# Optimization experiments

Hardware: AMD Instinct MI355X
Metric: run time of the kernel (lower is better)

The kernel has to match this reference:

```python
import jax, jax.numpy as jnp
import numpy as np

B, S, D, H, L, V = 2, 1024, 512, 8, 4, 32000
DK = D // H
EPS = 1e-6


def _positional_encoding():
    # row i of the original (d_model, seq) array: sin if i even else cos of t/10000^(2i/D); transposed -> (S, D)
    i = jnp.arange(D, dtype=jnp.float32)
    ang = jnp.arange(S, dtype=jnp.float32)[:, None] / (10000.0 ** (2.0 * i / D))[None, :]
    return jnp.where((jnp.arange(D) % 2 == 0)[None, :], jnp.sin(ang), jnp.cos(ang))


def _layernorm(x, g, b):
    m = jnp.mean(x, axis=-1, keepdims=True)
    s = jnp.std(x, axis=-1, keepdims=True)
    return g / (s + EPS) * (x - m) + b


def _mha(x, wq, wk, wv, wo, mask):
    # wq/wk/wv: [H, D, DK]; all heads batched via einsum (equivalent to per-head loop + concat)
    q = jnp.einsum('bsd,hdk->bhsk', x, wq)
    k = jnp.einsum('bsd,hdk->bhsk', x, wk)
    v = jnp.einsum('bsd,hdk->bhsk', x, wv)
    scores = jnp.einsum('bhsk,bhtk->bhst', q, k) / np.float32(np.sqrt(DK))
    if mask is not None:
        scores = scores + mask  # additive upper-tri 1e-15, faithful to source
    attn = jax.nn.softmax(scores, axis=-1)
    o = jnp.einsum('bhst,bhtv->bhsv', attn, v)
    o = o.transpose(0, 2, 1, 3).reshape(B, S, D)  # concat heads
    return o @ wo


def setup_inputs() -> dict:
    key = jax.random.key(0)
    ks = jax.random.split(key, 13)
    n = lambda k, shape, s=0.05: jax.random.normal(k, shape, dtype=jnp.float32) * s
    return {
        'tokens': jax.random.randint(ks[0], (B, S), 0, V),
        'emb': n(ks[1], (V, D)),
        'Wq': n(ks[2], (L, 2, H, D, DK)),
        'Wk': n(ks[3], (L, 2, H, D, DK)),
        'Wv': n(ks[4], (L, 2, H, D, DK)),
        'Wo': n(ks[5], (L, 2, D, D)),
        'ln_gain': 1.0 + n(ks[6], (L, 3, S, D)),
        'ln_bias': n(ks[7], (L, 3, S, D)),
        'ffn_w1': n(ks[8], (L, D, D)),
        'ffn_b1': n(ks[9], (L, D)),
        'ffn_w2': n(ks[10], (L, D, D)),
        'ffn_b2': n(ks[11], (L, D)),
    }


def reference(tokens, emb, Wq, Wk, Wv, Wo, ln_gain, ln_bias, ffn_w1, ffn_b1, ffn_w2, ffn_b2):
    pe = _positional_encoding()
    # NOTE: source applies sqrt(d_model) scalar AFTER adding positional encoding
    x = (emb[tokens] + pe[None, :, :]) * np.float32(np.sqrt(D))
    # source 'mask' adds 1e-15 to strictly-upper triangle (effectively a no-op; kept faithful)
    mask = (jnp.triu(jnp.ones((S, S), dtype=jnp.float32), 1) * 1e-15)[None, None, :, :]
    for l in range(L):
        h = _mha(x, Wq[l, 0], Wk[l, 0], Wv[l, 0], Wo[l, 0], mask)
        x = _layernorm(x + h, ln_gain[l, 0], ln_bias[l, 0])
        h = _mha(x, Wq[l, 1], Wk[l, 1], Wv[l, 1], Wo[l, 1], None)
        x = _layernorm(x + h, ln_gain[l, 1], ln_bias[l, 1])
        h = jax.nn.relu(x @ ffn_w1[l] + ffn_b1[l]) @ ffn_w2[l] + ffn_b2[l]
        x = _layernorm(x + h, ln_gain[l, 2], ln_bias[l, 2])
    # tied output projection with softmax (SharedWeights on transposed embedding)
    return jax.nn.softmax(x @ emb.T, axis=-1)
```

## Files before the change

### kernel.cpp

```cpp
#include <hip/hip_runtime.h>
#include <hip/hip_bf16.h>

typedef unsigned short u16;
typedef _Float16 f16x8 __attribute__((ext_vector_type(8)));
typedef float f32x4 __attribute__((ext_vector_type(4)));
typedef unsigned short u16x8 __attribute__((ext_vector_type(8)));

constexpr int kB = 2;
constexpr int kS = 1024;
constexpr int kD = 512;
constexpr int kH = 8;
constexpr int kDK = 64;
constexpr int kL = 4;
constexpr int kV = 32000;
constexpr int kM = kB * kS;
constexpr int kNB = kV / 128;

__device__ __forceinline__ u16 f2fh(float x) {
  _Float16 h = (_Float16)x;
  return __builtin_bit_cast(u16, h);
}
__device__ __forceinline__ float fh2f(u16 h) {
  return (float)__builtin_bit_cast(_Float16, h);
}
__device__ __forceinline__ u16 f2bh(float x) {
  unsigned u = __builtin_bit_cast(unsigned, x);
  unsigned r = u + 0x7fffu + ((u >> 16) & 1u);
  return (u16)(r >> 16);
}
__device__ __forceinline__ float bh2f(u16 h) {
  return __builtin_bit_cast(float, (unsigned)h << 16);
}
__device__ __forceinline__ void gload16(const u16* g, u16* l) {
  __builtin_amdgcn_global_load_lds(
      (const __attribute__((address_space(1))) unsigned int*)g,
      (__attribute__((address_space(3))) unsigned int*)l, 16, 0, 0);
}
__device__ __forceinline__ size_t swz_idx(int row, int k) {
  return (size_t)row * kD + (k & ~63) + ((((k >> 3) & 7) ^ (row & 7)) << 3) + (k & 7);
}

__global__ __launch_bounds__(256)
void conv_qkv(const float* __restrict__ Wq, const float* __restrict__ Wk,
              const float* __restrict__ Wv, u16* __restrict__ oh) {
  __shared__ float ld[64][65];
  const int kc = blockIdx.x, h = blockIdx.y, z = blockIdx.z;
  const int mat = z >> 3, lj = z & 7;
  const float* src = (mat == 0 ? Wq : mat == 1 ? Wk : Wv) +
                     ((size_t)(lj * kH + h)) * kD * kDK + (size_t)kc * 64 * kDK;
  const int t = threadIdx.x;
#pragma unroll
  for (int i = 0; i < 16; ++i) {
    const int idx = i * 256 + t;
    ld[idx >> 6][idx & 63] = src[idx];
  }
  __syncthreads();
  const int dkr = t >> 2, jb = t & 3;
  const size_t rowbase = ((size_t)lj * 1536 + mat * kD + h * kDK + dkr) * kD + kc * 64;
#pragma unroll
  for (int q = 0; q < 2; ++q) {
    const int jj = jb + q * 4;
    const int jsw = jj ^ (dkr & 7);
    u16x8 hi;
#pragma unroll
    for (int e = 0; e < 8; ++e) hi[e] = f2fh(ld[jj * 8 + e][dkr]);
    *(u16x8*)&oh[rowbase + jsw * 8] = hi;
  }
}

__global__ __launch_bounds__(256)
void conv_sq(const float* __restrict__ Wo, const float* __restrict__ w1,
             const float* __restrict__ w2, u16* __restrict__ woh,
             u16* __restrict__ w1h, u16* __restrict__ w2h) {
  __shared__ float ld[64][65];
  const int kc = blockIdx.x, nc = blockIdx.y, mid = blockIdx.z;
  const float* src;
  u16* dh;
  if (mid < 8) { src = Wo + (size_t)mid * kD * kD; dh = woh + (size_t)mid * kD * kD; }
  else if (mid < 12) { int l = mid - 8; src = w1 + (size_t)l * kD * kD; dh = w1h + (size_t)l * kD * kD; }
  else { int l = mid - 12; src = w2 + (size_t)l * kD * kD; dh = w2h + (size_t)l * kD * kD; }
  const int t = threadIdx.x;
#pragma unroll
  for (int i = 0; i < 16; ++i) {
    const int idx = i * 256 + t;
    const int kl = idx >> 6, nl = idx & 63;
    ld[kl][nl] = src[(size_t)(kc * 64 + kl) * kD + nc * 64 + nl];
  }
  __syncthreads();
  const int nr = t >> 2, jb = t & 3;
  const size_t rowbase = (size_t)(nc * 64 + nr) * kD + kc * 64;
#pragma unroll
  for (int q = 0; q < 2; ++q) {
    const int jj = jb + q * 4;
    const int jsw = jj ^ (nr & 7);
    u16x8 hi;
#pragma unroll
    for (int e = 0; e < 8; ++e) hi[e] = f2fh(ld[jj * 8 + e][nr]);
    *(u16x8*)&dh[rowbase + jsw * 8] = hi;
  }
}

__global__ __launch_bounds__(256)
void conv_emb(const float* __restrict__ emb, u16* __restrict__ oh) {
  const int chunk = blockIdx.x * 256 + threadIdx.x;
  const int n = chunk >> 6, j = chunk & 63;
  const float* s = &emb[(size_t)n * kD + j * 8];
  float4 a = *(const float4*)s, b = *(const float4*)(s + 4);
  u16x8 hi;
  hi[0] = f2fh(a.x); hi[1] = f2fh(a.y); hi[2] = f2fh(a.z); hi[3] = f2fh(a.w);
  hi[4] = f2fh(b.x); hi[5] = f2fh(b.y); hi[6] = f2fh(b.z); hi[7] = f2fh(b.w);
  *(u16x8*)&oh[(size_t)n * kD + (j & ~7) * 8 + (((j & 7) ^ (n & 7)) << 3)] = hi;
}

__global__ __launch_bounds__(256)
void embed_kernel(const int* __restrict__ tokens, const float* __restrict__ emb,
                  float* __restrict__ x, u16* __restrict__ xh) {
  const int row = blockIdx.x;
  const int s = row & (kS - 1);
  const int tok = tokens[row];
  const float scl = sqrtf((float)kD);
  for (int d = threadIdx.x; d < kD; d += 256) {
    float e = emb[(size_t)tok * kD + d];
    float den = powf(10000.0f, 2.0f * (float)d / (float)kD);
    float ang = (float)s / den;
    float pe = ((d & 1) == 0) ? sinf(ang) : cosf(ang);
    float o = (e + pe) * scl;
    x[(size_t)row * kD + d] = o;
    xh[swz_idx(row, d)] = f2fh(o);
  }
}

template <int BM, int BN, int OUT, int BIAS, int RELU>
__global__ __launch_bounds__(256)
void mgemm2(const u16* __restrict__ Ah, const u16* __restrict__ Bh,
            float* __restrict__ Cf, u16* __restrict__ Ch,
            const float* __restrict__ bias, float* __restrict__ partials,
            int Kd, int Nd) {
  static_assert(BM == BN, "");
  constexpr int MF = BM / 32, NF = BN / 32;
  constexpr int TA = BM * 64;
  constexpr int BUF = 2 * TA;
  __shared__ __align__(16) u16 lds[2 * BUF];
  __shared__ float plds[OUT == 3 ? 2 * BM : 1];
  const int t = threadIdx.x;
  const int lane = t & 63, g = lane >> 4, li = lane & 15;
  const int w = t >> 6, wr = w >> 1, wc = w & 1;
  const int m0 = blockIdx.x * BM, n0 = blockIdx.y * BN;

  f32x4 acc[MF][NF];
#pragma unroll
  for (int i = 0; i < MF; ++i)
#pragma unroll
    for (int j = 0; j < NF; ++j) acc[i][j] = (f32x4){0.f, 0.f, 0.f, 0.f};

  auto stage = [&](int c, int k0) {
    u16* base = &lds[c * BUF];
#pragma unroll
    for (int it = 0; it < BM / 32; ++it) {
      const int idx = it * 256 + t;
      const int r = idx >> 3, j = (idx & 7) * 8;
      gload16(&Ah[(size_t)(m0 + r) * Kd + k0 + j], &base[idx * 8]);
      gload16(&Bh[(size_t)(n0 + r) * Kd + k0 + j], &base[TA + idx * 8]);
    }
  };
  auto compute = [&](int c) {
    const u16* base = &lds[c * BUF];
#pragma unroll
    for (int s = 0; s < 2; ++s) {
      const int s4g = s * 4 + g;
      f16x8 fah[MF], fbh[NF];
#pragma unroll
      for (int fm = 0; fm < MF; ++fm) {
        const int row = wr * (BM / 2) + fm * 16 + li;
        fah[fm] = *(const f16x8*)&base[row * 64 + ((s4g ^ (row & 7)) << 3)];
      }
#pragma unroll
      for (int fn = 0; fn < NF; ++fn) {
        const int row = wc * (BN / 2) + fn * 16 + li;
        fbh[fn] = *(const f16x8*)&base[TA + row * 64 + ((s4g ^ (row & 7)) << 3)];
      }
#pragma unroll
      for (int fm = 0; fm < MF; ++fm)
#pragma unroll
        for (int fn = 0; fn < NF; ++fn)
          acc[fm][fn] = __builtin_amdgcn_mfma_f32_16x16x32_f16(
              fah[fm], fbh[fn], acc[fm][fn], 0, 0, 0);
    }
  };

  stage(0, 0);
  __syncthreads();
  int cur = 0;
  for (int k0 = 64; k0 < Kd; k0 += 64) {
    stage(cur ^ 1, k0);
    compute(cur);
    __syncthreads();
    cur ^= 1;
  }
  compute(cur);

#pragma unroll
  for (int fm = 0; fm < MF; ++fm)
#pragma unroll
    for (int fn = 0; fn < NF; ++fn)
#pragma unroll
      for (int r = 0; r < 4; ++r) {
        const int m = m0 + wr * (BM / 2) + fm * 16 + g * 4 + r;
        const int n = n0 + wc * (BN / 2) + fn * 16 + li;
        float c = acc[fm][fn][r];
        if (BIAS) c += bias[n];
        if (RELU) c = fmaxf(c, 0.0f);
        if (OUT == 0) {
          Cf[(size_t)m * Nd + n] = c;
        } else if (OUT == 1) {
          Ch[swz_idx(m, n)] = f2fh(c);
        } else if (OUT == 2) {
          const int mat = n >> 9, h = (n >> 6) & 7, dk = n & 63;
          const int b_ = m >> 10, s_ = m & (kS - 1);
          Ch[((size_t)mat * kM) * kD +
             (((size_t)(b_ * kH + h) * kS + s_) * kDK + dk)] = f2fh(c);
        } else {
          u16 q = f2bh(__expf(c));
          Ch[(size_t)m * Nd + n] = q;
          acc[fm][fn][r] = bh2f(q);
        }
      }
  if (OUT == 3) {
#pragma unroll
    for (int fm = 0; fm < MF; ++fm)
#pragma unroll
      for (int r = 0; r < 4; ++r) {
        float sv = 0.f;
#pragma unroll
        for (int fn = 0; fn < NF; ++fn) sv += acc[fm][fn][r];
        sv += __shfl_xor(sv, 1); sv += __shfl_xor(sv, 2);
        sv += __shfl_xor(sv, 4); sv += __shfl_xor(sv, 8);
        if (li == 0) plds[wc * BM + wr * (BM / 2) + fm * 16 + g * 4 + r] = sv;
      }
    __syncthreads();
    if (t < BM)
      partials[(size_t)(m0 + t) * gridDim.y + blockIdx.y] = plds[t] + plds[BM + t];
  }
}

__global__ __launch_bounds__(256)
void attn_kernel(const u16* __restrict__ qg, const u16* __restrict__ kg,
                 const u16* __restrict__ vg, u16* __restrict__ aoh) {
  __shared__ __align__(16) u16 Kt[2][2][64][40];
  __shared__ __align__(16) u16 Vt[2][2][64][40];
  __shared__ __align__(16) u16 Pt[2][64][40];
  const int t = threadIdx.x;
  const int lane = t & 63;
  const int g = lane >> 4, li = lane & 15;
  const int w = t >> 6;
  const int bh = blockIdx.y;
  const int q0 = blockIdx.x * 64;
  const size_t base = (size_t)bh * kS * kDK;
  const int r = t >> 2, dq = (t & 3) * 16;

  {
    const u16* src = &qg[base + (size_t)(q0 + r) * kDK + dq];
    u16x8 a = *(const u16x8*)src;
    u16x8 b = *(const u16x8*)(src + 8);
    *(u16x8*)&Pt[dq >> 5][r][dq & 31] = a;
    *(u16x8*)&Pt[dq >> 5][r][(dq & 31) + 8] = b;
  }
  __syncthreads();
  f16x8 qf0 = *(const f16x8*)&Pt[0][w * 16 + li][g * 8];
  f16x8 qf1 = *(const f16x8*)&Pt[1][w * 16 + li][g * 8];
  __syncthreads();

  float m_[4] = {-1e30f, -1e30f, -1e30f, -1e30f};
  float l_[4] = {0.f, 0.f, 0.f, 0.f};
  f32x4 apv[4];
#pragma unroll
  for (int i = 0; i < 4; ++i) apv[i] = (f32x4){0.f, 0.f, 0.f, 0.f};

  u16x8 ka, kb, va, vb;
  auto load_tile = [&](int kt) {
    const u16* ks = &kg[base + (size_t)(kt * 64 + r) * kDK + dq];
    ka = *(const u16x8*)ks;
    kb = *(const u16x8*)(ks + 8);
    const u16* vs = &vg[base + (size_t)(kt * 64 + r) * kDK + dq];
    va = *(const u16x8*)vs;
    vb = *(const u16x8*)(vs + 8);
  };
  auto store_tile = [&](int c) {
    *(u16x8*)&Kt[c][dq >> 5][r][dq & 31] = ka;
    *(u16x8*)&Kt[c][dq >> 5][r][(dq & 31) + 8] = kb;
    const int vc = r >> 5, ko = (r & 31) >> 3, kp = r & 7;
#pragma unroll
    for (int i = 0; i < 8; ++i) {
      const int d = dq + i;
      Vt[c][vc][d][((ko ^ (d >> 4)) << 3) | kp] = va[i];
    }
#pragma unroll
    for (int i = 0; i < 8; ++i) {
      const int d = dq + 8 + i;
      Vt[c][vc][d][((ko ^ (d >> 4)) << 3) | kp] = vb[i];
    }
  };

  load_tile(0);
  store_tile(0);
  for (int kt = 0; kt < kS / 64; ++kt) {
    const int c = kt & 1;
    if (kt < kS / 64 - 1) load_tile(kt + 1);
    __syncthreads();
    f32x4 s[4];
#pragma unroll
    for (int nf = 0; nf < 4; ++nf) {
      f16x8 k0 = *(const f16x8*)&Kt[c][0][nf * 16 + li][g * 8];
      f16x8 k1 = *(const f16x8*)&Kt[c][1][nf * 16 + li][g * 8];
      f32x4 sa = (f32x4){0.f, 0.f, 0.f, 0.f};
      sa = __builtin_amdgcn_mfma_f32_16x16x32_f16(qf0, k0, sa, 0, 0, 0);
      sa = __builtin_amdgcn_mfma_f32_16x16x32_f16(qf1, k1, sa, 0, 0, 0);
      s[nf] = sa;
    }
    float corr[4];
#pragma unroll
    for (int rr = 0; rr < 4; ++rr) {
      float tm = fmaxf(fmaxf(s[0][rr], s[1][rr]), fmaxf(s[2][rr], s[3][rr])) * 0.125f;
      tm = fmaxf(tm, __shfl_xor(tm, 1));
      tm = fmaxf(tm, __shfl_xor(tm, 2));
      tm = fmaxf(tm, __shfl_xor(tm, 4));
      tm = fmaxf(tm, __shfl_xor(tm, 8));
      const float nm = fmaxf(m_[rr], tm);
      corr[rr] = __expf(m_[rr] - nm);
      m_[rr] = nm;
    }
    float tsum[4] = {0.f, 0.f, 0.f, 0.f};
    u16 pb[4][4];
#pragma unroll
    for (int nf = 0; nf < 4; ++nf)
#pragma unroll
      for (int rr = 0; rr < 4; ++rr) {
        float p = __expf(s[nf][rr] * 0.125f - m_[rr]);
        tsum[rr] += p;
        pb[nf][rr] = f2fh(p);
      }
#pragma unroll
    for (int rr = 0; rr < 4; ++rr) {
      float ts = tsum[rr];
      ts += __shfl_xor(ts, 1); ts += __shfl_xor(ts, 2);
      ts += __shfl_xor(ts, 4); ts += __shfl_xor(ts, 8);
      l_[rr] = l_[rr] * corr[rr] + ts;
#pragma unroll
      for (int nf = 0; nf < 4; ++nf) apv[nf][rr] *= corr[rr];
    }
#pragma unroll
    for (int nf = 0; nf < 4; ++nf)
#pragma unroll
      for (int rr = 0; rr < 4; ++rr)
        Pt[nf >> 1][w * 16 + g * 4 + rr][(nf & 1) * 16 + li] = pb[nf][rr];
    f16x8 p0 = *(const f16x8*)&Pt[0][w * 16 + li][g * 8];
    f16x8 p1 = *(const f16x8*)&Pt[1][w * 16 + li][g * 8];
#pragma unroll
    for (int nf = 0; nf < 4; ++nf) {
      f16x8 v0 = *(const f16x8*)&Vt[c][0][nf * 16 + li][((g ^ nf) & 3) * 8];
      f16x8 v1 = *(const f16x8*)&Vt[c][1][nf * 16 + li][((g ^ nf) & 3) * 8];
      apv[nf] = __builtin_amdgcn_mfma_f32_16x16x32_f16(p0, v0, apv[nf], 0, 0, 0);
      apv[nf] = __builtin_amdgcn_mfma_f32_16x16x32_f16(p1, v1, apv[nf], 0, 0, 0);
    }
    if (kt < kS / 64 - 1) store_tile(c ^ 1);
  }
  const int b_ = bh >> 3, h_ = bh & 7;
#pragma unroll
  for (int rr = 0; rr < 4; ++rr) {
    const float inv = 1.0f / l_[rr];
    const int row = q0 + w * 16 + g * 4 + rr;
    const int m = b_ * kS + row;
#pragma unroll
    for (int nf = 0; nf < 4; ++nf) {
      const int d = h_ * kDK + nf * 16 + li;
      aoh[swz_idx(m, d)] = f2fh(apv[nf][rr] * inv);
    }
  }
}

__global__ __launch_bounds__(256)
void ln_kernel(float* __restrict__ x, const float* __restrict__ h,
               const float* __restrict__ gain, const float* __restrict__ bias,
               u16* __restrict__ xh) {
  const int row = blockIdx.x;
  const int s = row & (kS - 1);
  const int t = threadIdx.x;
  float* xr = x + (size_t)row * kD;
  const float* hr = h + (size_t)row * kD;
  const float v0 = xr[t] + hr[t];
  const float v1 = xr[t + 256] + hr[t + 256];
  float sum = v0 + v1;
  float sq = v0 * v0 + v1 * v1;
#pragma unroll
  for (int off = 1; off < 64; off <<= 1) {
    sum += __shfl_xor(sum, off);
    sq += __shfl_xor(sq, off);
  }
  __shared__ float rs[4], rq[4];
  if ((t & 63) == 0) { rs[t >> 6] = sum; rq[t >> 6] = sq; }
  __syncthreads();
  sum = rs[0] + rs[1] + rs[2] + rs[3];
  sq = rq[0] + rq[1] + rq[2] + rq[3];
  const float mean = sum * (1.0f / kD);
  const float var = fmaxf(sq * (1.0f / kD) - mean * mean, 0.0f);
  const float inv = 1.0f / (sqrtf(var) + 1e-6f);
  const float* gr = gain + (size_t)s * kD;
  const float* br = bias + (size_t)s * kD;
  const float o0 = gr[t] * inv * (v0 - mean) + br[t];
  const float o1 = gr[t + 256] * inv * (v1 - mean) + br[t + 256];
  xr[t] = o0;
  xr[t + 256] = o1;
  xh[swz_idx(row, t)] = f2fh(o0);
  xh[swz_idx(row, t + 256)] = f2fh(o1);
}

__global__ __launch_bounds__(256)
void scale_kernel(const u16* __restrict__ expb, const float* __restrict__ partials,
                  float* __restrict__ out) {
  const int row = blockIdx.x;
  const int t = threadIdx.x;
  float s = (t < kNB) ? partials[(size_t)row * kNB + t] : 0.f;
#pragma unroll
  for (int off = 1; off < 64; off <<= 1) s += __shfl_xor(s, off);
  __shared__ float red[4];
  if ((t & 63) == 0) red[t >> 6] = s;
  __syncthreads();
  const float inv = 1.0f / (red[0] + red[1] + red[2] + red[3]);
  const u16x8* src = (const u16x8*)(expb + (size_t)row * kV);
  float4* dst = (float4*)(out + (size_t)row * kV);
  for (int i = t; i < kV / 8; i += 256) {
    u16x8 v = src[i];
    float4 a = make_float4(bh2f(v[0]) * inv, bh2f(v[1]) * inv,
                           bh2f(v[2]) * inv, bh2f(v[3]) * inv);
    float4 b = make_float4(bh2f(v[4]) * inv, bh2f(v[5]) * inv,
                           bh2f(v[6]) * inv, bh2f(v[7]) * inv);
    dst[i * 2] = a;
    dst[i * 2 + 1] = b;
  }
}

extern "C" void kernel_launch(void* const* d_in, const int* in_sizes, int n_in,
                              void* d_out, int out_size, void* d_ws, size_t ws_size,
                              hipStream_t stream) {
  (void)in_sizes; (void)n_in; (void)out_size; (void)ws_size;
  const int* tokens = (const int*)d_in[0];
  const float* emb = (const float*)d_in[1];
  const float* Wq = (const float*)d_in[2];
  const float* Wk = (const float*)d_in[3];
  const float* Wv = (const float*)d_in[4];
  const float* Wo = (const float*)d_in[5];
  const float* lng = (const float*)d_in[6];
  const float* lnb = (const float*)d_in[7];
  const float* w1 = (const float*)d_in[8];
  const float* b1 = (const float*)d_in[9];
  const float* w2 = (const float*)d_in[10];
  const float* b2 = (const float*)d_in[11];

  size_t off = 0;
  auto alloc = [&](size_t bytes) {
    void* p = (char*)d_ws + off;
    off += (bytes + 255) & ~(size_t)255;
    return p;
  };
  const size_t NA = (size_t)kM * kD;
  float* x = (float*)alloc(NA * 4);
  u16* xh = (u16*)alloc(NA * 2);
  u16* qkvb = (u16*)alloc(3 * NA * 2);
  u16* aoh = (u16*)alloc(NA * 2);
  float* t1 = (float*)alloc(NA * 4);
  u16* t1h = (u16*)alloc(NA * 2);
  float* ao2 = (float*)alloc(NA * 4);
  float* partials = (float*)alloc((size_t)kM * kNB * 4);
  u16* expb = (u16*)alloc((size_t)kM * kV * 2);
  u16* wqkvh = (u16*)alloc((size_t)8 * 1536 * kD * 2);
  u16* woh = (u16*)alloc((size_t)8 * kD * kD * 2);
  u16* w1h = (u16*)alloc((size_t)4 * kD * kD * 2);
  u16* w2h = (u16*)alloc((size_t)4 * kD * kD * 2);
  u16* embh = (u16*)alloc((size_t)kV * kD * 2);

  conv_qkv<<<dim3(8, 8, 24), 256, 0, stream>>>(Wq, Wk, Wv, wqkvh);
  conv_sq<<<dim3(8, 8, 16), 256, 0, stream>>>(Wo, w1, w2, woh, w1h, w2h);
  conv_emb<<<kV * kD / 8 / 256, 256, 0, stream>>>(emb, embh);
  embed_kernel<<<kM, 256, 0, stream>>>(tokens, emb, x, xh);

  for (int l = 0; l < kL; ++l) {
    for (int j = 0; j < 2; ++j) {
      const size_t lj = (size_t)(l * 2 + j);
      mgemm2<128, 128, 2, 0, 0><<<dim3(kM / 128, 12), 256, 0, stream>>>(
          xh, wqkvh + lj * 1536 * kD, nullptr, qkvb, nullptr, nullptr, kD, 1536);
      attn_kernel<<<dim3(kS / 64, kB * kH), 256, 0, stream>>>(
          qkvb, qkvb + NA, qkvb + 2 * NA, aoh);
      mgemm2<64, 64, 0, 0, 0><<<dim3(kM / 64, kD / 64), 256, 0, stream>>>(
          aoh, woh + lj * kD * kD, t1, nullptr, nullptr, nullptr, kD, kD);
      ln_kernel<<<kM, 256, 0, stream>>>(x, t1, lng + (size_t)(l * 3 + j) * kS * kD,
                                        lnb + (size_t)(l * 3 + j) * kS * kD, xh);
    }
    mgemm2<64, 64, 1, 1, 1><<<dim3(kM / 64, kD / 64), 256, 0, stream>>>(
        xh, w1h + (size_t)l * kD * kD, nullptr, t1h, b1 + (size_t)l * kD,
        nullptr, kD, kD);
    mgemm2<64, 64, 0, 1, 0><<<dim3(kM / 64, kD / 64), 256, 0, stream>>>(
        t1h, w2h + (size_t)l * kD * kD, ao2, nullptr, b2 + (size_t)l * kD,
        nullptr, kD, kD);
    ln_kernel<<<kM, 256, 0, stream>>>(x, ao2, lng + (size_t)(l * 3 + 2) * kS * kD,
                                      lnb + (size_t)(l * 3 + 2) * kS * kD, xh);
  }
  mgemm2<128, 128, 3, 0, 0><<<dim3(kM / 128, kNB), 256, 0, stream>>>(
      xh, embh, nullptr, expb, nullptr, partials, kD, kV);
  scale_kernel<<<kM, 256, 0, stream>>>(expb, partials, (float*)d_out);
}
```

Measured before the change: 669.4 us.

## Transpose V in QKV epilogue, drop attention LDS staging, pack LN params, remap vocab grid

The QKV GEMM now writes V transposed (d-major per head) through an LDS transpose, so the attention kernel reads K and V fragments straight from global memory and no longer stages them in LDS or synchronises per tile. Q fragments are also loaded directly. LayerNorm gain and bias are pre-packed into interleaved fp16 pairs to halve parameter traffic. The vocab projection uses a 1D grid with an XCD-aware block remap to improve L2 locality of the embedding tiles. The trade-offs are more global/L2 traffic in attention, fp16 precision loss on the LN parameters, and an extra conversion pass.

```diff
diff --git a/kernel.cpp b/kernel.cpp
--- a/kernel.cpp
+++ b/kernel.cpp
@@ -5,6 +5,7 @@
 typedef _Float16 f16x8 __attribute__((ext_vector_type(8)));
 typedef float f32x4 __attribute__((ext_vector_type(4)));
 typedef unsigned short u16x8 __attribute__((ext_vector_type(8)));
+typedef unsigned int u32x4 __attribute__((ext_vector_type(4)));
 
 constexpr int kB = 2;
 constexpr int kS = 1024;
@@ -110,6 +111,25 @@
   hi[0] = f2fh(a.x); hi[1] = f2fh(a.y); hi[2] = f2fh(a.z); hi[3] = f2fh(a.w);
   hi[4] = f2fh(b.x); hi[5] = f2fh(b.y); hi[6] = f2fh(b.z); hi[7] = f2fh(b.w);
   *(u16x8*)&oh[(size_t)n * kD + (j & ~7) * 8 + (((j & 7) ^ (n & 7)) << 3)] = hi;
+}
+
+__global__ __launch_bounds__(256)
+void conv_gb(const float* __restrict__ g, const float* __restrict__ b,
+             unsigned* __restrict__ out) {
+  const size_t e0 = ((size_t)blockIdx.x * 256 + threadIdx.x) * 8;
+  float4 ga = *(const float4*)&g[e0], gc = *(const float4*)&g[e0 + 4];
+  float4 ba = *(const float4*)&b[e0], bc = *(const float4*)&b[e0 + 4];
+  u32x4 o0, o1;
+  o0[0] = (unsigned)f2fh(ga.x) | ((unsigned)f2fh(ba.x) << 16);
+  o0[1] = (unsigned)f2fh(ga.y) | ((unsigned)f2fh(ba.y) << 16);
+  o0[2] = (unsigned)f2fh(ga.z) | ((unsigned)f2fh(ba.z) << 16);
+  o0[3] = (unsigned)f2fh(ga.w) | ((unsigned)f2fh(ba.w) << 16);
+  o1[0] = (unsigned)f2fh(gc.x) | ((unsigned)f2fh(bc.x) << 16);
+  o1[1] = (unsigned)f2fh(gc.y) | ((unsigned)f2fh(bc.y) << 16);
+  o1[2] = (unsigned)f2fh(gc.z) | ((unsigned)f2fh(bc.z) << 16);
+  o1[3] = (unsigned)f2fh(gc.w) | ((unsigned)f2fh(bc.w) << 16);
+  *(u32x4*)&out[e0] = o0;
+  *(u32x4*)&out[e0 + 4] = o1;
 }
 
 __global__ __launch_bounds__(256)
@@ -130,7 +150,7 @@
   }
 }
 
-template <int BM, int BN, int OUT, int BIAS, int RELU>
+template <int BM, int BN, int OUT, int BIAS, int RELU, int XSW = 0>
 __global__ __launch_bounds__(256)
 void mgemm2(const u16* __restrict__ Ah, const u16* __restrict__ Bh,
             float* __restrict__ Cf, u16* __restrict__ Ch,
@@ -145,7 +165,19 @@
   const int t = threadIdx.x;
   const int lane = t & 63, g = lane >> 4, li = lane & 15;
   const int w = t >> 6, wr = w >> 1, wc = w & 1;
-  const int m0 = blockIdx.x * BM, n0 = blockIdx.y * BN;
+  int m0, n0, nidx;
+  if (XSW) {
+    const int phys = blockIdx.x;
+    const int cpx = gridDim.x >> 3;
+    const int lin = (phys & 7) * cpx + (phys >> 3);
+    m0 = (lin & (kM / BM - 1)) * BM;
+    nidx = lin / (kM / BM);
+    n0 = nidx * BN;
+  } else {
+    m0 = blockIdx.x * BM;
+    nidx = blockIdx.y;
+    n0 = nidx * BN;
+  }
 
   f32x4 acc[MF][NF];
 #pragma unroll
@@ -199,6 +231,7 @@
   }
   compute(cur);
 
+  const int vmat = (OUT == 2) ? (n0 >> 9) : 0;
 #pragma unroll
   for (int fm = 0; fm < MF; ++fm)
 #pragma unroll
@@ -215,16 +248,47 @@
         } else if (OUT == 1) {
           Ch[swz_idx(m, n)] = f2fh(c);
         } else if (OUT == 2) {
-          const int mat = n >> 9, h = (n >> 6) & 7, dk = n & 63;
-          const int b_ = m >> 10, s_ = m & (kS - 1);
-          Ch[((size_t)mat * kM) * kD +
-             (((size_t)(b_ * kH + h) * kS + s_) * kDK + dk)] = f2fh(c);
+          if (vmat < 2) {
+            const int h = (n >> 6) & 7, dk = n & 63;
+            const int b_ = m >> 10, s_ = m & (kS - 1);
+            Ch[(size_t)vmat * kM * kD +
+               (((size_t)(b_ * kH + h) * kS + s_) * kDK + dk)] = f2fh(c);
+          }
         } else {
           u16 q = f2bh(__expf(c));
           Ch[(size_t)m * Nd + n] = q;
           acc[fm][fn][r] = bh2f(q);
         }
       }
+  if (OUT == 2 && vmat == 2) {
+    u16* ldsT = lds;
+    constexpr int TS = BM + 2;
+    __syncthreads();
+#pragma unroll
+    for (int fm = 0; fm < MF; ++fm)
+#pragma unroll
+      for (int fn = 0; fn < NF; ++fn)
+#pragma unroll
+        for (int r = 0; r < 4; ++r) {
+          const int ml = wr * (BM / 2) + fm * 16 + g * 4 + r;
+          const int nl = wc * (BN / 2) + fn * 16 + li;
+          ldsT[nl * TS + ml] = f2fh(acc[fm][fn][r]);
+        }
+    __syncthreads();
+    const int b_ = m0 >> 10;
+    const int s0_ = m0 & (kS - 1);
+#pragma unroll
+    for (int rep = 0; rep < BM * BN / 256 / 8; ++rep) {
+      const int idx = rep * 256 + t;
+      const int nl = idx >> (31 - __builtin_clz(BM / 8));
+      const int c8 = (idx & (BM / 8 - 1)) * 8;
+      const int nn = n0 + nl;
+      const int h = (nn >> 6) & 7, dk = nn & 63;
+      u16x8 v = *(const u16x8*)&ldsT[nl * TS + c8];
+      *(u16x8*)&Ch[2 * (size_t)kM * kD +
+                   ((size_t)(b_ * kH + h) * kDK + dk) * kS + s0_ + c8] = v;
+    }
+  }
   if (OUT == 3) {
 #pragma unroll
     for (int fm = 0; fm < MF; ++fm)
@@ -239,15 +303,13 @@
       }
     __syncthreads();
     if (t < BM)
-      partials[(size_t)(m0 + t) * gridDim.y + blockIdx.y] = plds[t] + plds[BM + t];
+      partials[(size_t)(m0 + t) * (Nd / BN) + nidx] = plds[t] + plds[BM + t];
   }
 }
 
 __global__ __launch_bounds__(256)
 void attn_kernel(const u16* __restrict__ qg, const u16* __restrict__ kg,
-                 const u16* __restrict__ vg, u16* __restrict__ aoh) {
-  __shared__ __align__(16) u16 Kt[2][2][64][40];
-  __shared__ __align__(16) u16 Vt[2][2][64][40];
+                 const u16* __restrict__ vtg, u16* __restrict__ aoh) {
   __shared__ __align__(16) u16 Pt[2][64][40];
   const int t = threadIdx.x;
   const int lane = t & 63;
@@ -256,19 +318,10 @@
   const int bh = blockIdx.y;
   const int q0 = blockIdx.x * 64;
   const size_t base = (size_t)bh * kS * kDK;
-  const int r = t >> 2, dq = (t & 3) * 16;
-
-  {
-    const u16* src = &qg[base + (size_t)(q0 + r) * kDK + dq];
-    u16x8 a = *(const u16x8*)src;
-    u16x8 b = *(const u16x8*)(src + 8);
-    *(u16x8*)&Pt[dq >> 5][r][dq & 31] = a;
-    *(u16x8*)&Pt[dq >> 5][r][(dq & 31) + 8] = b;
-  }
-  __syncthreads();
-  f16x8 qf0 = *(const f16x8*)&Pt[0][w * 16 + li][g * 8];
-  f16x8 qf1 = *(const f16x8*)&Pt[1][w * 16 + li][g * 8];
-  __syncthreads();
+  const size_t vbase = (size_t)bh * kDK * kS;
+  const int qrow = q0 + w * 16 + li;
+  const f16x8 qf0 = *(const f16x8*)&qg[base + (size_t)qrow * kDK + g * 8];
+  const f16x8 qf1 = *(const f16x8*)&qg[base + (size_t)qrow * kDK + 32 + g * 8];
 
   float m_[4] = {-1e30f, -1e30f, -1e30f, -1e30f};
   float l_[4] = {0.f, 0.f, 0.f, 0.f};
@@ -276,42 +329,14 @@
 #pragma unroll
   for (int i = 0; i < 4; ++i) apv[i] = (f32x4){0.f, 0.f, 0.f, 0.f};
 
-  u16x8 ka, kb, va, vb;
-  auto load_tile = [&](int kt) {
-    const u16* ks = &kg[base + (size_t)(kt * 64 + r) * kDK + dq];
-    ka = *(const u16x8*)ks;
-    kb = *(const u16x8*)(ks + 8);
-    const u16* vs = &vg[base + (size_t)(kt * 64 + r) * kDK + dq];
-    va = *(const u16x8*)vs;
-    vb = *(const u16x8*)(vs + 8);
-  };
-  auto store_tile = [&](int c) {
-    *(u16x8*)&Kt[c][dq >> 5][r][dq & 31] = ka;
-    *(u16x8*)&Kt[c][dq >> 5][r][(dq & 31) + 8] = kb;
-    const int vc = r >> 5, ko = (r & 31) >> 3, kp = r & 7;
-#pragma unroll
-    for (int i = 0; i < 8; ++i) {
-      const int d = dq + i;
-      Vt[c][vc][d][((ko ^ (d >> 4)) << 3) | kp] = va[i];
-    }
-#pragma unroll
-    for (int i = 0; i < 8; ++i) {
-      const int d = dq + 8 + i;
-      Vt[c][vc][d][((ko ^ (d >> 4)) << 3) | kp] = vb[i];
-    }
-  };
-
-  load_tile(0);
-  store_tile(0);
+#pragma unroll 2
   for (int kt = 0; kt < kS / 64; ++kt) {
-    const int c = kt & 1;
-    if (kt < kS / 64 - 1) load_tile(kt + 1);
-    __syncthreads();
     f32x4 s[4];
 #pragma unroll
     for (int nf = 0; nf < 4; ++nf) {
-      f16x8 k0 = *(const f16x8*)&Kt[c][0][nf * 16 + li][g * 8];
-      f16x8 k1 = *(const f16x8*)&Kt[c][1][nf * 16 + li][g * 8];
+      const size_t krow = base + (size_t)(kt * 64 + nf * 16 + li) * kDK;
+      const f16x8 k0 = *(const f16x8*)&kg[krow + g * 8];
+      const f16x8 k1 = *(const f16x8*)&kg[krow + 32 + g * 8];
       f32x4 sa = (f32x4){0.f, 0.f, 0.f, 0.f};
       sa = __builtin_amdgcn_mfma_f32_16x16x32_f16(qf0, k0, sa, 0, 0, 0);
       sa = __builtin_amdgcn_mfma_f32_16x16x32_f16(qf1, k1, sa, 0, 0, 0);
@@ -353,16 +378,16 @@
 #pragma unroll
       for (int rr = 0; rr < 4; ++rr)
         Pt[nf >> 1][w * 16 + g * 4 + rr][(nf & 1) * 16 + li] = pb[nf][rr];
-    f16x8 p0 = *(const f16x8*)&Pt[0][w * 16 + li][g * 8];
-    f16x8 p1 = *(const f16x8*)&Pt[1][w * 16 + li][g * 8];
+    const f16x8 p0 = *(const f16x8*)&Pt[0][w * 16 + li][g * 8];
+    const f16x8 p1 = *(const f16x8*)&Pt[1][w * 16 + li][g * 8];
 #pragma unroll
     for (int nf = 0; nf < 4; ++nf) {
-      f16x8 v0 = *(const f16x8*)&Vt[c][0][nf * 16 + li][((g ^ nf) & 3) * 8];
-      f16x8 v1 = *(const f16x8*)&Vt[c][1][nf * 16 + li][((g ^ nf) & 3) * 8];
+      const size_t vrow = vbase + (size_t)(nf * 16 + li) * kS + kt * 64;
+      const f16x8 v0 = *(const f16x8*)&vtg[vrow + g * 8];
+      const f16x8 v1 = *(const f16x8*)&vtg[vrow + 32 + g * 8];
       apv[nf] = __builtin_amdgcn_mfma_f32_16x16x32_f16(p0, v0, apv[nf], 0, 0, 0);
       apv[nf] = __builtin_amdgcn_mfma_f32_16x16x32_f16(p1, v1, apv[nf], 0, 0, 0);
     }
-    if (kt < kS / 64 - 1) store_tile(c ^ 1);
   }
   const int b_ = bh >> 3, h_ = bh & 7;
 #pragma unroll
@@ -380,8 +405,7 @@
 
 __global__ __launch_bounds__(256)
 void ln_kernel(float* __restrict__ x, const float* __restrict__ h,
-               const float* __restrict__ gain, const float* __restrict__ bias,
-               u16* __restrict__ xh) {
+               const unsigned* __restrict__ gb, u16* __restrict__ xh) {
   const int row = blockIdx.x;
   const int s = row & (kS - 1);
   const int t = threadIdx.x;
@@ -404,10 +428,10 @@
   const float mean = sum * (1.0f / kD);
   const float var = fmaxf(sq * (1.0f / kD) - mean * mean, 0.0f);
   const float inv = 1.0f / (sqrtf(var) + 1e-6f);
-  const float* gr = gain + (size_t)s * kD;
-  const float* br = bias + (size_t)s * kD;
-  const float o0 = gr[t] * inv * (v0 - mean) + br[t];
-  const float o1 = gr[t + 256] * inv * (v1 - mean) + br[t + 256];
+  const unsigned* gbr = gb + (size_t)s * kD;
+  const unsigned p0 = gbr[t], p1 = gbr[t + 256];
+  const float o0 = fh2f((u16)p0) * inv * (v0 - mean) + fh2f((u16)(p0 >> 16));
+  const float o1 = fh2f((u16)p1) * inv * (v1 - mean) + fh2f((u16)(p1 >> 16));
   xr[t] = o0;
   xr[t + 256] = o1;
   xh[swz_idx(row, t)] = f2fh(o0);
@@ -477,10 +501,12 @@
   u16* w1h = (u16*)alloc((size_t)4 * kD * kD * 2);
   u16* w2h = (u16*)alloc((size_t)4 * kD * kD * 2);
   u16* embh = (u16*)alloc((size_t)kV * kD * 2);
+  unsigned* gb = (unsigned*)alloc((size_t)kL * 3 * kS * kD * 4);
 
   conv_qkv<<<dim3(8, 8, 24), 256, 0, stream>>>(Wq, Wk, Wv, wqkvh);
   conv_sq<<<dim3(8, 8, 16), 256, 0, stream>>>(Wo, w1, w2, woh, w1h, w2h);
   conv_emb<<<kV * kD / 8 / 256, 256, 0, stream>>>(emb, embh);
+  conv_gb<<<kL * 3 * kS * kD / 8 / 256, 256, 0, stream>>>(lng, lnb, gb);
   embed_kernel<<<kM, 256, 0, stream>>>(tokens, emb, x, xh);
 
   for (int l = 0; l < kL; ++l) {
@@ -492,8 +518,7 @@
           qkvb, qkvb + NA, qkvb + 2 * NA, aoh);
       mgemm2<64, 64, 0, 0, 0><<<dim3(kM / 64, kD / 64), 256, 0, stream>>>(
           aoh, woh + lj * kD * kD, t1, nullptr, nullptr, nullptr, kD, kD);
-      ln_kernel<<<kM, 256, 0, stream>>>(x, t1, lng + (size_t)(l * 3 + j) * kS * kD,
-                                        lnb + (size_t)(l * 3 + j) * kS * kD, xh);
+      ln_kernel<<<kM, 256, 0, stream>>>(x, t1, gb + (size_t)(l * 3 + j) * kS * kD, xh);
     }
     mgemm2<64, 64, 1, 1, 1><<<dim3(kM / 64, kD / 64), 256, 0, stream>>>(
         xh, w1h + (size_t)l * kD * kD, nullptr, t1h, b1 + (size_t)l * kD,
@@ -501,10 +526,9 @@
     mgemm2<64, 64, 0, 1, 0><<<dim3(kM / 64, kD / 64), 256, 0, stream>>>(
         t1h, w2h + (size_t)l * kD * kD, ao2, nullptr, b2 + (size_t)l * kD,
         nullptr, kD, kD);
-    ln_kernel<<<kM, 256, 0, stream>>>(x, ao2, lng + (size_t)(l * 3 + 2) * kS * kD,
-                                      lnb + (size_t)(l * 3 + 2) * kS * kD, xh);
-  }
-  mgemm2<128, 128, 3, 0, 0><<<dim3(kM / 128, kNB), 256, 0, stream>>>(
+    ln_kernel<<<kM, 256, 0, stream>>>(x, ao2, gb + (size_t)(l * 3 + 2) * kS * kD, xh);
+  }
+  mgemm2<128, 128, 3, 0, 0, 1><<<dim3(kM / 128 * kNB), 256, 0, stream>>>(
       xh, embh, nullptr, expb, nullptr, partials, kD, kV);
   scale_kernel<<<kM, 256, 0, stream>>>(expb, partials, (float*)d_out);
 }
```

After: 868.5 us. +29.7%, slower.
